# Kernel optimization log

Measured on AMD Instinct MI355X. Metric: run time of the kernel, lower is better.

The kernel has to match this reference:

```python
import jax, jax.numpy as jnp
import numpy as np

VOCAB, EMB = 100000, 128
KERNEL_NUM, SIGMA, EXACT_SIGMA = 21, 0.1, 0.001
OUT_LAYERS = [10, 5]

def _mus_sigmas():
    step = 2.0 / (KERNEL_NUM - 1)
    mus = [1.0, 1.0 - step / 2]
    for i in range(1, KERNEL_NUM - 1):
        mus.append(mus[i] - step)
    mus = list(reversed(mus))  # [-0.95, ..., 0.95, 1.0]
    sigmas = [SIGMA] * (KERNEL_NUM - 1) + [EXACT_SIGMA]
    return mus, sigmas

MUS, SIGMAS = _mus_sigmas()

def setup_inputs() -> dict:
    key = jax.random.key(0)
    ks = jax.random.split(key, 12)
    B, Q, D = 1024, 64, 256
    q1 = jax.random.randint(ks[0], (B, Q), 0, VOCAB, dtype=jnp.int32)
    d1 = jax.random.randint(ks[1], (B, D), 0, VOCAB, dtype=jnp.int32)
    q2 = jax.random.randint(ks[2], (B, Q), 0, VOCAB, dtype=jnp.int32)
    d2 = jax.random.randint(ks[3], (B, D), 0, VOCAB, dtype=jnp.int32)
    emb = jax.random.normal(ks[4], (VOCAB, EMB), dtype=jnp.float32)
    emb = emb.at[0].set(0.0)  # padding_idx=0
    dims = [KERNEL_NUM] + OUT_LAYERS + [1]
    W1 = jax.random.normal(ks[5], (dims[0], dims[1]), dtype=jnp.float32) / np.sqrt(dims[0])
    b1 = jnp.zeros((dims[1],), dtype=jnp.float32)
    W2 = jax.random.normal(ks[6], (dims[1], dims[2]), dtype=jnp.float32) / np.sqrt(dims[1])
    b2 = jnp.zeros((dims[2],), dtype=jnp.float32)
    W3 = jax.random.normal(ks[7], (dims[2], dims[3]), dtype=jnp.float32) / np.sqrt(dims[2])
    b3 = jnp.zeros((dims[3],), dtype=jnp.float32)
    return {"q1": q1, "d1": d1, "q2": q2, "d2": d2, "emb": emb,
            "W1": W1, "b1": b1, "W2": W2, "b2": b2, "W3": W3, "b3": b3}

def _matching_matrix(emb, q_ids, d_ids):
    q = emb[q_ids]  # [B,Q,E]
    d = emb[d_ids]  # [B,D,E]
    qn = q / (jnp.linalg.norm(q, axis=-1, keepdims=True) + 1e-13)
    dn = d / (jnp.linalg.norm(d, axis=-1, keepdims=True) + 1e-13)
    return jnp.einsum('bqe,bde->bqd', qn, dn)  # [B,Q,D]

def _apply_kernels(M):
    KM = []
    for mu, sig in zip(MUS, SIGMAS):
        k = jnp.exp(-(M - mu) ** 2 / (2.0 * sig ** 2))
        KM.append(jnp.log1p(k.sum(axis=-1)).sum(axis=-1))  # [B]
    return jnp.stack(KM, axis=-1)  # [B,21]

def _mlp(x, W1, b1, W2, b2, W3, b3):
    # _get_mlp puts ReLU BEFORE each Linear
    x = jax.nn.relu(x) @ W1 + b1
    x = jax.nn.relu(x) @ W2 + b2
    x = jax.nn.relu(x) @ W3 + b3
    return x  # [B,1]

def _predict(emb, q, d, W1, b1, W2, b2, W3, b3):
    M = _matching_matrix(emb, q, d)
    ko = _apply_kernels(M)
    return _mlp(ko, W1, b1, W2, b2, W3, b3)

def reference(q1, d1, q2, d2, emb, W1, b1, W2, b2, W3, b3):
    l1 = _predict(emb, q1, d1, W1, b1, W2, b2, W3, b3)
    l2 = _predict(emb, q2, d2, W1, b1, W2, b2, W3, b3)
    return jax.nn.sigmoid(l1 - l2)  # [B,1]
```

## Files before the change

### kernel.cpp

```cpp
#include <hip/hip_runtime.h>


typedef __attribute__((ext_vector_type(8))) _Float16 f16x8;
typedef __attribute__((ext_vector_type(4))) float f32x4;
typedef __attribute__((ext_vector_type(2))) float f32x2;

__device__ __forceinline__ unsigned short h2s(_Float16 h) {
    return __builtin_bit_cast(unsigned short, h);
}

__global__ __launch_bounds__(256)
void norm_split_kernel(const float* __restrict__ emb,
                       unsigned short* __restrict__ tab, int vocab)
{
    const int row = blockIdx.x * 8 + (threadIdx.x >> 5);
    if (row >= vocab) return;
    const int ln = threadIdx.x & 31;
    const float4 v = *reinterpret_cast<const float4*>(emb + (size_t)row * 128 + ln * 4);
    float ss = v.x*v.x + v.y*v.y + v.z*v.z + v.w*v.w;
    #pragma unroll
    for (int m = 16; m >= 1; m >>= 1) ss += __shfl_xor(ss, m);
    const float rn = 1.0f / (sqrtf(ss) + 1e-13f);
    const unsigned short h0 = h2s((_Float16)(v.x * rn));
    const unsigned short h1 = h2s((_Float16)(v.y * rn));
    const unsigned short h2 = h2s((_Float16)(v.z * rn));
    const unsigned short h3 = h2s((_Float16)(v.w * rn));
    *reinterpret_cast<uint2*>(tab + (size_t)row * 128 + ln * 4) =
        make_uint2((unsigned)h0 | ((unsigned)h1 << 16), (unsigned)h2 | ((unsigned)h3 << 16));
}

__device__ __forceinline__ void glds16(const unsigned short* g, unsigned short* l) {
    __builtin_amdgcn_global_load_lds((const __attribute__((address_space(1))) void*)g,
                                     (__attribute__((address_space(3))) void*)l, 16, 0, 0);
}

__device__ __forceinline__ void stage_d16(const unsigned short* __restrict__ tab,
                                          const int* __restrict__ ids, int base,
                                          unsigned short* __restrict__ db,
                                          int w, int l)
{
    const int r   = 4*w + (l >> 4);
    const int id  = ids[base + r];
    const int gsw = ((l & 15) ^ r) << 3;
    glds16(tab + (size_t)id * 128 + gsw, db + 4*w * 128);
}

__device__ __forceinline__ void stage_q16(const unsigned short* __restrict__ tab,
                                          const int* __restrict__ qids,
                                          unsigned short* __restrict__ db,
                                          int w, int l)
{
    #pragma unroll
    for (int j = 0; j < 4; j++) {
        const int r   = 4*j + (l >> 4);
        const int id  = qids[16*w + r];
        const int gsw = ((l & 15) ^ r) << 3;
        glds16(tab + (size_t)id * 128 + gsw, db + 4*j * 128);
    }
}

__device__ __constant__ float KC[21] = {
    2.8625185805e-20f, 2.3195228302e-16f, 6.9144001069e-13f, 7.5825604279e-10f,
    3.0590232050e-7f,  4.5399929762e-5f,  2.4787521767e-3f,  4.9787068368e-2f,
    3.6787944117e-1f,  1.0f,              1.0f,              3.6787944117e-1f,
    4.9787068368e-2f,  2.4787521767e-3f,  4.5399929762e-5f,  3.0590232050e-7f,
    7.5825604279e-10f, 6.9144001069e-13f, 2.3195228302e-16f, 2.8625185805e-20f,
    1.0f
};

__device__ __forceinline__ void apply_pair(float m0, float m1, f32x2 (&sp)[21]) {
    const f32x2 m2 = {m0, m1};
    const f32x2 dm = m2 - 0.05f;
    const f32x2 ta = (dm * dm) * -72.13475204444817f;
    const f32x2 x2 = m2 * 14.426950408889634f;
    const f32x2 t0 = { __builtin_amdgcn_exp2f(ta[0]), __builtin_amdgcn_exp2f(ta[1]) };
    const f32x2 R  = { __builtin_amdgcn_exp2f(x2[0]), __builtin_amdgcn_exp2f(x2[1]) };
    const f32x2 Ri = { __builtin_amdgcn_exp2f(-x2[0]), __builtin_amdgcn_exp2f(-x2[1]) };
    sp[10] += t0;
    f32x2 tu = t0;
    tu *= R;  sp[11] += tu;
    tu *= R;  sp[12] += tu;
    tu *= R;  sp[13] += tu;
    tu *= R;  sp[14] += tu;
    tu *= R;  sp[15] += tu;
    tu *= R;  sp[16] += tu;
    tu *= R;  sp[17] += tu;
    tu *= R;  sp[18] += tu;
    tu *= R;  sp[19] += tu;
    f32x2 td = t0;
    td *= Ri; sp[9] += td;
    td *= Ri; sp[8] += td;
    td *= Ri; sp[7] += td;
    td *= Ri; sp[6] += td;
    td *= Ri; sp[5] += td;
    td *= Ri; sp[4] += td;
    td *= Ri; sp[3] += td;
    td *= Ri; sp[2] += td;
    td *= Ri; sp[1] += td;
    td *= Ri; sp[0] += td;
    const f32x2 e  = m2 - 1.0f;
    const f32x2 ea = (e * e) * -721347.5204444817f;
    const f32x2 ex = { __builtin_amdgcn_exp2f(ea[0]), __builtin_amdgcn_exp2f(ea[1]) };
    sp[20] += ex;
}

__global__ __launch_bounds__(256, 2)
void knrm_main(const int* __restrict__ q1, const int* __restrict__ d1,
               const int* __restrict__ q2, const int* __restrict__ d2,
               const unsigned short* __restrict__ tab,
               float* __restrict__ kmws)
{
    __shared__ unsigned short buf[6][16*128];
    __shared__ int   sh_ids[256];
    __shared__ float KMpart[4][21];

    const int tid = threadIdx.x;
    const int bb  = blockIdx.x >> 1;
    const int p   = blockIdx.x & 1;
    const int w   = tid >> 6;
    const int l   = tid & 63;
    const int lr  = l & 15;
    const int lh  = l >> 4;

    const int* qids = (p == 0 ? q1 : q2) + bb * 64;
    const int* dids = (p == 0 ? d1 : d2) + bb * 256;

    sh_ids[tid] = dids[tid];
    stage_q16(tab, qids, buf[w], w, l);
    asm volatile("s_waitcnt vmcnt(0) lgkmcnt(0)" ::: "memory");
    __builtin_amdgcn_s_barrier();

    f16x8 Bq[4];
    #pragma unroll
    for (int ks = 0; ks < 4; ks++) {
        const int off = lr*128 + (((ks*4 + lh) ^ lr) << 3);
        Bq[ks] = *reinterpret_cast<const f16x8*>(&buf[w][off]);
    }
    asm volatile("s_waitcnt lgkmcnt(0)" ::: "memory");
    __builtin_amdgcn_s_barrier();

    f32x2 sp[21];
    #pragma unroll
    for (int i = 0; i < 21; i++) sp[i] = (f32x2){0.f, 0.f};

    stage_d16(tab, sh_ids, 0,  buf[0], w, l);
    stage_d16(tab, sh_ids, 16, buf[1], w, l);
    stage_d16(tab, sh_ids, 32, buf[2], w, l);
    stage_d16(tab, sh_ids, 48, buf[3], w, l);
    stage_d16(tab, sh_ids, 64, buf[4], w, l);

    for (int c = 0; c < 16; c++) {
        if (c <= 11)      asm volatile("s_waitcnt vmcnt(4)" ::: "memory");
        else if (c == 12) asm volatile("s_waitcnt vmcnt(3)" ::: "memory");
        else if (c == 13) asm volatile("s_waitcnt vmcnt(2)" ::: "memory");
        else if (c == 14) asm volatile("s_waitcnt vmcnt(1)" ::: "memory");
        else              asm volatile("s_waitcnt vmcnt(0)" ::: "memory");
        __builtin_amdgcn_s_barrier();

        const unsigned short* cb = buf[c % 6];
        f32x4 C = {0.f,0.f,0.f,0.f};
        #pragma unroll
        for (int ks = 0; ks < 4; ks++) {
            const int o = lr*128 + (((ks*4 + lh) ^ lr) << 3);
            const f16x8 A = *reinterpret_cast<const f16x8*>(cb + o);
            C = __builtin_amdgcn_mfma_f32_16x16x32_f16(A, Bq[ks], C, 0, 0, 0);
        }
        apply_pair(C[0], C[1], sp);
        apply_pair(C[2], C[3], sp);

        if (c <= 10)
            stage_d16(tab, sh_ids, (c + 5) * 16, buf[(c + 5) % 6], w, l);
    }

    #pragma unroll
    for (int i = 0; i < 21; i++) {
        float s = (sp[i][0] + sp[i][1]) * KC[i];
        s += __shfl_xor(s, 16);
        s += __shfl_xor(s, 32);
        float t = log1pf(s);
        t += __shfl_xor(t, 1);
        t += __shfl_xor(t, 2);
        t += __shfl_xor(t, 4);
        t += __shfl_xor(t, 8);
        if (l == 0) KMpart[w][i] = t;
    }
    __syncthreads();
    if (tid < 21)
        kmws[blockIdx.x * 21 + tid] = KMpart[0][tid] + KMpart[1][tid]
                                    + KMpart[2][tid] + KMpart[3][tid];
}

__global__ __launch_bounds__(64)
void mlp_kernel(const float* __restrict__ kmws,
                const float* __restrict__ W1, const float* __restrict__ b1,
                const float* __restrict__ W2, const float* __restrict__ b2,
                const float* __restrict__ W3, const float* __restrict__ b3,
                float* __restrict__ out)
{
    __shared__ float KMs[2][21], x1s[2][10], x2s[2][5];
    const int tid = threadIdx.x;
    const int bb  = blockIdx.x;
    if (tid < 42) KMs[tid / 21][tid % 21] = kmws[(bb * 2 + tid / 21) * 21 + (tid % 21)];
    __syncthreads();
    if (tid < 10) {
        for (int p = 0; p < 2; p++) {
            float acc = b1[tid];
            #pragma unroll
            for (int i = 0; i < 21; i++) acc = fmaf(fmaxf(KMs[p][i], 0.0f), W1[i*10 + tid], acc);
            x1s[p][tid] = acc;
        }
    }
    __syncthreads();
    if (tid < 5) {
        for (int p = 0; p < 2; p++) {
            float acc = b2[tid];
            #pragma unroll
            for (int i = 0; i < 10; i++) acc = fmaf(fmaxf(x1s[p][i], 0.0f), W2[i*5 + tid], acc);
            x2s[p][tid] = acc;
        }
    }
    __syncthreads();
    if (tid == 0) {
        float lv[2];
        for (int p = 0; p < 2; p++) {
            float acc = b3[0];
            #pragma unroll
            for (int i = 0; i < 5; i++) acc = fmaf(fmaxf(x2s[p][i], 0.0f), W3[i], acc);
            lv[p] = acc;
        }
        out[bb] = 1.0f / (1.0f + expf(lv[1] - lv[0]));
    }
}

typedef __attribute__((ext_vector_type(8))) short bf16x8;
__device__ __forceinline__ unsigned short f2bf(float f) {
    unsigned u = __float_as_uint(f);
    u += 0x7fffu + ((u >> 16) & 1u);
    return (unsigned short)(u >> 16);
}
__device__ __forceinline__ float bf2f(unsigned short h) {
    return __uint_as_float(((unsigned)h) << 16);
}
__device__ __forceinline__ void stage_f32(const float* __restrict__ emb,
                                          const int* __restrict__ ids,
                                          unsigned short* __restrict__ hi,
                                          unsigned short* __restrict__ lo,
                                          int tid)
{
    const int lg = tid >> 5;
    const int ln = tid & 31;
    #pragma unroll
    for (int i = 0; i < 4; i++) {
        const int row = i * 8 + lg;
        const int id  = ids[row];
        const float4 v = *reinterpret_cast<const float4*>(emb + (size_t)id * 128 + ln * 4);
        float ss = v.x*v.x + v.y*v.y + v.z*v.z + v.w*v.w;
        #pragma unroll
        for (int m = 16; m >= 1; m >>= 1) ss += __shfl_xor(ss, m);
        const float rn = 1.0f / (sqrtf(ss) + 1e-13f);
        const float f0 = v.x*rn, f1 = v.y*rn, f2 = v.z*rn, f3 = v.w*rn;
        const unsigned short h0 = f2bf(f0), h1 = f2bf(f1), h2 = f2bf(f2), h3 = f2bf(f3);
        const unsigned short g0 = f2bf(f0 - bf2f(h0)), g1 = f2bf(f1 - bf2f(h1));
        const unsigned short g2 = f2bf(f2 - bf2f(h2)), g3 = f2bf(f3 - bf2f(h3));
        const int off = row*128 + (((ln >> 1) ^ (row & 15)) << 3) + ((ln & 1) << 2);
        *reinterpret_cast<uint2*>(hi + off) =
            make_uint2((unsigned)h0 | ((unsigned)h1 << 16), (unsigned)h2 | ((unsigned)h3 << 16));
        *reinterpret_cast<uint2*>(lo + off) =
            make_uint2((unsigned)g0 | ((unsigned)g1 << 16), (unsigned)g2 | ((unsigned)g3 << 16));
    }
}
#define MFMB(a, b, c) __builtin_amdgcn_mfma_f32_16x16x32_bf16((a), (b), (c), 0, 0, 0)

__global__ __launch_bounds__(256, 2)
void knrm_fallback(const int* __restrict__ q1, const int* __restrict__ d1,
                   const int* __restrict__ q2, const int* __restrict__ d2,
                   const float* __restrict__ emb,
                   const float* __restrict__ W1, const float* __restrict__ b1,
                   const float* __restrict__ W2, const float* __restrict__ b2,
                   const float* __restrict__ W3, const float* __restrict__ b3,
                   float* __restrict__ out)
{
    __shared__ unsigned short bh[2][32*128], bl[2][32*128];
    __shared__ float KMpart[2][4][21];
    __shared__ float x1s[2][10], x2s[2][5];
    const int tid = threadIdx.x;
    const int bb  = blockIdx.x;
    const int w   = tid >> 6;
    const int l   = tid & 63;
    const int lr  = l & 15;
    const int lh  = l >> 4;

    for (int p = 0; p < 2; p++) {
        const int* qids = (p == 0 ? q1 : q2) + bb * 64;
        const int* dids = (p == 0 ? d1 : d2) + bb * 256;
        stage_f32(emb, qids,      bh[0], bl[0], tid);
        stage_f32(emb, qids + 32, bh[1], bl[1], tid);
        __syncthreads();
        bf16x8 Bh[4], Bl[4];
        const int qb = w >> 1;
        const int qr = (w * 16 + lr) & 31;
        #pragma unroll
        for (int ks = 0; ks < 4; ks++) {
            const int off = qr*128 + (((ks*4 + lh) ^ lr) << 3);
            Bh[ks] = *reinterpret_cast<const bf16x8*>(&bh[qb][off]);
            Bl[ks] = *reinterpret_cast<const bf16x8*>(&bl[qb][off]);
        }
        __syncthreads();
        f32x2 sp[21];
        #pragma unroll
        for (int i = 0; i < 21; i++) sp[i] = (f32x2){0.f, 0.f};
        for (int c = 0; c < 8; c++) {
            stage_f32(emb, dids + c * 32, bh[c & 1], bl[c & 1], tid);
            __syncthreads();
            const unsigned short* ch = bh[c & 1];
            const unsigned short* cl = bl[c & 1];
            f32x4 C0 = {0.f,0.f,0.f,0.f}, C1 = {0.f,0.f,0.f,0.f};
            #pragma unroll
            for (int ks = 0; ks < 4; ks++) {
                const int o0 = lr*128        + (((ks*4 + lh) ^ lr) << 3);
                const int o1 = (16 + lr)*128 + (((ks*4 + lh) ^ lr) << 3);
                const bf16x8 A0h = *reinterpret_cast<const bf16x8*>(ch + o0);
                const bf16x8 A0l = *reinterpret_cast<const bf16x8*>(cl + o0);
                const bf16x8 A1h = *reinterpret_cast<const bf16x8*>(ch + o1);
                const bf16x8 A1l = *reinterpret_cast<const bf16x8*>(cl + o1);
                C0 = MFMB(A0h, Bh[ks], C0); C1 = MFMB(A1h, Bh[ks], C1);
                C0 = MFMB(A0h, Bl[ks], C0); C1 = MFMB(A1h, Bl[ks], C1);
                C0 = MFMB(A0l, Bh[ks], C0); C1 = MFMB(A1l, Bh[ks], C1);
            }
            apply_pair(C0[0], C0[1], sp); apply_pair(C0[2], C0[3], sp);
            apply_pair(C1[0], C1[1], sp); apply_pair(C1[2], C1[3], sp);
            __syncthreads();
        }
        #pragma unroll
        for (int i = 0; i < 21; i++) {
            float s = (sp[i][0] + sp[i][1]) * KC[i];
            s += __shfl_xor(s, 16);
            s += __shfl_xor(s, 32);
            float t = log1pf(s);
            t += __shfl_xor(t, 1);
            t += __shfl_xor(t, 2);
            t += __shfl_xor(t, 4);
            t += __shfl_xor(t, 8);
            if (l == 0) KMpart[p][w][i] = t;
        }
    }
    __syncthreads();
    if (tid < 10) {
        for (int p = 0; p < 2; p++) {
            float acc = b1[tid];
            #pragma unroll
            for (int i = 0; i < 21; i++) {
                const float km = KMpart[p][0][i] + KMpart[p][1][i]
                               + KMpart[p][2][i] + KMpart[p][3][i];
                acc = fmaf(fmaxf(km, 0.0f), W1[i*10 + tid], acc);
            }
            x1s[p][tid] = acc;
        }
    }
    __syncthreads();
    if (tid < 5) {
        for (int p = 0; p < 2; p++) {
            float acc = b2[tid];
            #pragma unroll
            for (int i = 0; i < 10; i++) acc = fmaf(fmaxf(x1s[p][i], 0.0f), W2[i*5 + tid], acc);
            x2s[p][tid] = acc;
        }
    }
    __syncthreads();
    if (tid == 0) {
        float lv[2];
        for (int p = 0; p < 2; p++) {
            float acc = b3[0];
            #pragma unroll
            for (int i = 0; i < 5; i++) acc = fmaf(fmaxf(x2s[p][i], 0.0f), W3[i], acc);
            lv[p] = acc;
        }
        out[bb] = 1.0f / (1.0f + expf(lv[1] - lv[0]));
    }
}

extern "C" void kernel_launch(void* const* d_in, const int* in_sizes, int n_in,
                              void* d_out, int out_size, void* d_ws, size_t ws_size,
                              hipStream_t stream)
{
    const int*   q1  = (const int*)  d_in[0];
    const int*   d1  = (const int*)  d_in[1];
    const int*   q2  = (const int*)  d_in[2];
    const int*   d2  = (const int*)  d_in[3];
    const float* emb = (const float*)d_in[4];
    const float* W1  = (const float*)d_in[5];
    const float* b1  = (const float*)d_in[6];
    const float* W2  = (const float*)d_in[7];
    const float* b2  = (const float*)d_in[8];
    const float* W3  = (const float*)d_in[9];
    const float* b3  = (const float*)d_in[10];
    float* out = (float*)d_out;
    (void)n_in;

    const int    vocab = in_sizes[4] / 128;
    const size_t tabsz = (size_t)vocab * 128 * 2;
    const size_t kmsz  = (size_t)out_size * 2 * 21 * 4;
    const size_t need  = tabsz + kmsz;

    if (ws_size >= need) {
        unsigned short* tab = (unsigned short*)d_ws;
        float* kmws = (float*)((char*)d_ws + tabsz);
        norm_split_kernel<<<(vocab + 7) / 8, 256, 0, stream>>>(emb, tab, vocab);
        knrm_main<<<out_size * 2, 256, 0, stream>>>(q1, d1, q2, d2, tab, kmws);
        mlp_kernel<<<out_size, 64, 0, stream>>>(kmws, W1, b1, W2, b2, W3, b3, out);
    } else {
        knrm_fallback<<<out_size, 256, 0, stream>>>(q1, d1, q2, d2, emb,
                                                    W1, b1, W2, b2, W3, b3, out);
    }
}
```

Measured before the change: 104.6 us.

## Skip exact-match kernel exp when no score nears one; pipeline MFMA with kernel apply

The exact-match Gaussian (sigma 0.001) is now evaluated only when some wave lane has a similarity above 0.98. Below that threshold the term underflows to zero in float, so the result is unchanged and most exp2 calls for that kernel are removed. The main loop is also software-pipelined: it computes the MFMA for the next chunk while the soft-bin accumulation is applied to the previous chunk's results, so matrix and vector work can overlap. The cost is an extra wave-wide vote plus a branch per chunk, and one more accumulator tile kept live in registers.

```diff
diff --git a/kernel.cpp b/kernel.cpp
--- a/kernel.cpp
+++ b/kernel.cpp
@@ -68,7 +68,7 @@
     1.0f
 };
 
-__device__ __forceinline__ void apply_pair(float m0, float m1, f32x2 (&sp)[21]) {
+__device__ __forceinline__ void apply_pair_g(float m0, float m1, f32x2 (&sp)[21]) {
     const f32x2 m2 = {m0, m1};
     const f32x2 dm = m2 - 0.05f;
     const f32x2 ta = (dm * dm) * -72.13475204444817f;
@@ -98,10 +98,21 @@
     td *= Ri; sp[2] += td;
     td *= Ri; sp[1] += td;
     td *= Ri; sp[0] += td;
-    const f32x2 e  = m2 - 1.0f;
-    const f32x2 ea = (e * e) * -721347.5204444817f;
-    const f32x2 ex = { __builtin_amdgcn_exp2f(ea[0]), __builtin_amdgcn_exp2f(ea[1]) };
-    sp[20] += ex;
+}
+
+__device__ __forceinline__ void apply_chunk(const f32x4& C, f32x2 (&sp)[21]) {
+    apply_pair_g(C[0], C[1], sp);
+    apply_pair_g(C[2], C[3], sp);
+    const float cmax = fmaxf(fmaxf(C[0], C[1]), fmaxf(C[2], C[3]));
+    if (__any(cmax > 0.98f)) {
+        const f32x2 e0 = { C[0] - 1.0f, C[1] - 1.0f };
+        const f32x2 e1 = { C[2] - 1.0f, C[3] - 1.0f };
+        const f32x2 a0 = (e0 * e0) * -721347.5204444817f;
+        const f32x2 a1 = (e1 * e1) * -721347.5204444817f;
+        const f32x2 ex = { __builtin_amdgcn_exp2f(a0[0]) + __builtin_amdgcn_exp2f(a1[0]),
+                           __builtin_amdgcn_exp2f(a0[1]) + __builtin_amdgcn_exp2f(a1[1]) };
+        sp[20] += ex;
+    }
 }
 
 __global__ __launch_bounds__(256, 2)
@@ -149,7 +160,18 @@
     stage_d16(tab, sh_ids, 48, buf[3], w, l);
     stage_d16(tab, sh_ids, 64, buf[4], w, l);
 
-    for (int c = 0; c < 16; c++) {
+    f32x4 Cp = {0.f,0.f,0.f,0.f};
+    asm volatile("s_waitcnt vmcnt(4)" ::: "memory");
+    __builtin_amdgcn_s_barrier();
+    #pragma unroll
+    for (int ks = 0; ks < 4; ks++) {
+        const int o = lr*128 + (((ks*4 + lh) ^ lr) << 3);
+        const f16x8 A = *reinterpret_cast<const f16x8*>(buf[0] + o);
+        Cp = __builtin_amdgcn_mfma_f32_16x16x32_f16(A, Bq[ks], Cp, 0, 0, 0);
+    }
+    stage_d16(tab, sh_ids, 80, buf[5], w, l);
+
+    for (int c = 1; c < 16; c++) {
         if (c <= 11)      asm volatile("s_waitcnt vmcnt(4)" ::: "memory");
         else if (c == 12) asm volatile("s_waitcnt vmcnt(3)" ::: "memory");
         else if (c == 13) asm volatile("s_waitcnt vmcnt(2)" ::: "memory");
@@ -165,12 +187,13 @@
             const f16x8 A = *reinterpret_cast<const f16x8*>(cb + o);
             C = __builtin_amdgcn_mfma_f32_16x16x32_f16(A, Bq[ks], C, 0, 0, 0);
         }
-        apply_pair(C[0], C[1], sp);
-        apply_pair(C[2], C[3], sp);
-
         if (c <= 10)
             stage_d16(tab, sh_ids, (c + 5) * 16, buf[(c + 5) % 6], w, l);
-    }
+
+        apply_chunk(Cp, sp);
+        Cp = C;
+    }
+    apply_chunk(Cp, sp);
 
     #pragma unroll
     for (int i = 0; i < 21; i++) {
@@ -327,8 +350,8 @@
                 C0 = MFMB(A0h, Bl[ks], C0); C1 = MFMB(A1h, Bl[ks], C1);
                 C0 = MFMB(A0l, Bh[ks], C0); C1 = MFMB(A1l, Bh[ks], C1);
             }
-            apply_pair(C0[0], C0[1], sp); apply_pair(C0[2], C0[3], sp);
-            apply_pair(C1[0], C1[1], sp); apply_pair(C1[2], C1[3], sp);
+            apply_chunk(C0, sp);
+            apply_chunk(C1, sp);
             __syncthreads();
         }
         #pragma unroll
```

Result: faster. 101.3 us (-3.1%).
